# Kernel optimization log

Hardware: AMD Instinct MI355X
Metric: run time of the kernel (lower is better)

## Reference

```python
import jax, jax.numpy as jnp
import numpy as np

GAMMA = 1.0  # init arg gamma


def setup_inputs() -> dict:
    key = jax.random.key(0)
    ks = jax.random.split(key, 7)
    Bn, C, C_, H = 8, 256, 32, 64
    sc = 1.0 / np.sqrt(C)
    return {
        "x_activation": jax.random.normal(ks[0], (Bn, C, H, H), dtype=jnp.float32),
        "f_w": jax.random.normal(ks[1], (C_, C), dtype=jnp.float32) * sc,
        "f_b": jnp.zeros((C_,), dtype=jnp.float32),
        "g_w": jax.random.normal(ks[2], (C_, C), dtype=jnp.float32) * sc,
        "g_b": jnp.zeros((C_,), dtype=jnp.float32),
        "h_w": jax.random.normal(ks[3], (C, C), dtype=jnp.float32) * sc,
        "h_b": jnp.zeros((C,), dtype=jnp.float32),
    }


def reference(x_activation, f_w, f_b, g_w, g_b, h_w, h_b):
    Bn, C, H, W = x_activation.shape
    N = H * W
    xf = x_activation.reshape(Bn, C, N)  # [B, C, N]
    # 1x1 convs are per-pixel linear maps over channels
    f = jnp.einsum('oc,bcn->bon', f_w, xf) + f_b[:, None]  # [B, C_, N]
    g = jnp.einsum('oc,bcn->bon', g_w, xf) + g_b[:, None]  # [B, C_, N]
    h = jnp.einsum('oc,bcn->bon', h_w, xf) + h_b[:, None]  # [B, C, N]
    # S[b, i, j] = sum_c f[b, c, i] * g[b, c, j]  (f^T @ g), shape [B, N, N]
    S = jnp.einsum('bci,bcj->bij', f, g)
    # NOTE: original uses Softmax(dim=1) -> normalize over the i (query/f) axis
    B = jax.nn.softmax(S, axis=1)
    # O (post-transpose) [b, c, i] = sum_j B[b, i, j] * h[b, c, j]
    O = jnp.einsum('bij,bcj->bci', B, h).reshape(Bn, C, H, W)
    return GAMMA * O + x_activation
```

## Files before the change

### kernel.cpp

```cpp
#include <hip/hip_runtime.h>
#include <hip/hip_fp16.h>
#include <cmath>


#define BN 8
#define CC 256
#define CQ 32
#define NN 4096

typedef _Float16 half8 __attribute__((ext_vector_type(8)));
typedef _Float16 half4v __attribute__((ext_vector_type(4)));
typedef float f32x4 __attribute__((ext_vector_type(4)));

static __device__ __forceinline__ float fexp2(float x) {
    return __builtin_amdgcn_exp2f(x);
}

#define LOG2E 1.44269504f
#define SHIFT2 28.8539008f

__global__ __launch_bounds__(256) void transpose_kernel(
    const float* __restrict__ x, __half* __restrict__ xt,
    const float* __restrict__ fw, const float* __restrict__ gw,
    const float* __restrict__ hw, __half* __restrict__ wf16)
{
    const int gid = blockIdx.x;

    if (gid >= 2048) {
        int i = (gid - 2048) * 256 + threadIdx.x;
        float v;
        if (i < 8192)       v = fw[i];
        else if (i < 16384) v = gw[i - 8192];
        else                v = hw[i - 16384];
        wf16[i] = __float2half(v);
        return;
    }

    const int b = gid & 7, rest = gid >> 3;
    const int n0 = (rest & 63) * 64;
    const int c0 = (rest >> 6) * 64;
    const int tid = threadIdx.x;

    __shared__ float T[64 * 65];

    const float* xb = x + ((size_t)b * CC + c0) * NN + n0;
    const int u  = tid >> 4;
    const int n4 = (tid & 15) * 4;
#pragma unroll
    for (int r = 0; r < 4; ++r) {
        int c = r * 16 + u;
        f32x4 v = __builtin_nontemporal_load((const f32x4*)(xb + (size_t)c * NN + n4));
        T[c * 65 + n4 + 0] = v.x;
        T[c * 65 + n4 + 1] = v.y;
        T[c * 65 + n4 + 2] = v.z;
        T[c * 65 + n4 + 3] = v.w;
    }
    __syncthreads();

    const int lane = tid & 63, w = tid >> 6;
    const int n  = w * 16 + (lane >> 2);
    const int cc = (lane & 3) * 16;
    half8 o0, o1;
#pragma unroll
    for (int k = 0; k < 8; ++k) {
        o0[k] = (_Float16)T[(cc + k) * 65 + n];
        o1[k] = (_Float16)T[(cc + 8 + k) * 65 + n];
    }
    __half* dst = xt + ((size_t)b * NN + n0 + n) * CC + c0 + cc;
    *(half8*)(void*)dst = o0;
    *(half8*)(void*)(dst + 8) = o1;
}

__global__ __launch_bounds__(256) void proj_kernel(
    const __half* __restrict__ xt, const __half* __restrict__ wf16,
    const float* __restrict__ fb, const float* __restrict__ gb,
    const float* __restrict__ hb,
    __half* __restrict__ ft, __half* __restrict__ gt, __half* __restrict__ hm)
{
    const int tid = threadIdx.x;
    const int w = tid >> 6, lane = tid & 63, col = lane & 15, q = lane >> 4;
    const int gid = blockIdx.x;
    const int b = gid & 7, rest = gid >> 3;
    const int n0 = (rest & 63) * 64;
    const int ot = rest >> 6;

    const __half* xtb  = xt + (size_t)b * NN * CC;
    const __half* fw16 = wf16;
    const __half* gw16 = wf16 + 8192;
    const __half* hw16 = wf16 + 16384;

    f32x4 acc[4];
#pragma unroll
    for (int mt = 0; mt < 4; ++mt) acc[mt] = (f32x4){0.f, 0.f, 0.f, 0.f};

    if (ot == 0) {
        const int pix = n0 + 16 * w + col;
#pragma unroll
        for (int ks = 0; ks < 8; ++ks) {
            half8 bf = *(const half8*)(const void*)(xtb + (size_t)pix * CC + ks * 32 + q * 8);
#pragma unroll
            for (int mt = 0; mt < 4; ++mt) {
                const __half* wp = (mt < 2) ? (fw16 + (16 * mt + col) * CC)
                                            : (gw16 + (16 * (mt - 2) + col) * CC);
                half8 af = *(const half8*)(const void*)(wp + ks * 32 + q * 8);
                acc[mt] = __builtin_amdgcn_mfma_f32_16x16x32_f16(af, bf, acc[mt], 0, 0, 0);
            }
        }
#pragma unroll
        for (int mt = 0; mt < 4; ++mt) {
            const int mtl = mt & 1;
            const float* bsel = (mt < 2) ? fb : gb;
            __half* dsel = (mt < 2) ? ft : gt;
            half4v hv;
#pragma unroll
            for (int r = 0; r < 4; ++r)
                hv[r] = (_Float16)(acc[mt][r] + bsel[16 * mtl + 4 * q + r]);
            *(half4v*)(void*)(dsel + ((size_t)b * NN + pix) * CQ + 16 * mtl + 4 * q) = hv;
        }
    } else {
        const int c = (ot - 1) * 64 + 16 * w + col;
#pragma unroll
        for (int ks = 0; ks < 8; ++ks) {
            half8 bf = *(const half8*)(const void*)(hw16 + (size_t)c * CC + ks * 32 + q * 8);
#pragma unroll
            for (int mt = 0; mt < 4; ++mt) {
                half8 af = *(const half8*)(const void*)(xtb + (size_t)(n0 + 16 * mt + col) * CC + ks * 32 + q * 8);
                acc[mt] = __builtin_amdgcn_mfma_f32_16x16x32_f16(af, bf, acc[mt], 0, 0, 0);
            }
        }
        const float bias = hb[c];
#pragma unroll
        for (int mt = 0; mt < 4; ++mt) {
            half4v hv;
#pragma unroll
            for (int r = 0; r < 4; ++r)
                hv[r] = (_Float16)(acc[mt][r] + bias);
            *(half4v*)(void*)(hm + ((size_t)b * CC + c) * NN + n0 + 16 * mt + 4 * q) = hv;
        }
    }
}

__global__ __launch_bounds__(256) void pass1_kernel(
    const __half* __restrict__ ft, const __half* __restrict__ gt,
    float* __restrict__ shl)
{
    const int tid = threadIdx.x;
    const int w = tid >> 6, lane = tid & 63, col = lane & 15, q = lane >> 4;
    const int gid = blockIdx.x;
    const int b = gid & 7;
    const int jg = (gid >> 3) * 64 + 16 * w + col;

    const __half* fbase = ft + (size_t)b * NN * CQ;
    half8 gfrag = *(const half8*)(const void*)(gt + ((size_t)b * NN + jg) * CQ + q * 8);

    float a0 = 0.f, a1 = 0.f, a2 = 0.f, a3 = 0.f;
    const f32x4 zero = {0.f, 0.f, 0.f, 0.f};

    half8 a_cur = *(const half8*)(const void*)(fbase + (size_t)col * CQ + q * 8);
    for (int i0 = 0; i0 < NN; i0 += 16) {
        int i_n = (i0 + 16) & (NN - 1);
        half8 a_next = *(const half8*)(const void*)(fbase + (size_t)(i_n + col) * CQ + q * 8);
        f32x4 d = __builtin_amdgcn_mfma_f32_16x16x32_f16(a_cur, gfrag, zero, 0, 0, 0);
        a0 += fexp2(fmaf(d[0], LOG2E, -SHIFT2));
        a1 += fexp2(fmaf(d[1], LOG2E, -SHIFT2));
        a2 += fexp2(fmaf(d[2], LOG2E, -SHIFT2));
        a3 += fexp2(fmaf(d[3], LOG2E, -SHIFT2));
        a_cur = a_next;
    }
    float l = (a0 + a1) + (a2 + a3);
    l += __shfl_xor(l, 16);
    l += __shfl_xor(l, 32);
    if (q == 0)
        shl[(size_t)b * NN + jg] = -__log2f(l) - SHIFT2;
}

__global__ __launch_bounds__(512, 4) void pass2_kernel(
    const float* __restrict__ x,
    const __half* __restrict__ ft, const __half* __restrict__ gt,
    const __half* __restrict__ hm, const float* __restrict__ shl,
    float* __restrict__ out)
{
    const int tid = threadIdx.x;
    const int w = tid >> 6, lane = tid & 63, col = lane & 15, q = lane >> 4;
    const int gid = blockIdx.x;
    const int b  = gid & 7;
    const int i0 = (gid >> 3) * 64;
    const int sg  = w >> 2;
    const int sw4 = w & 3;
    const int cb  = 32 * w;

    __shared__ __half P[2][64 * 64];

    const __half* gbase = gt + (size_t)b * NN * CQ;
    const __half* hbase = hm + (size_t)b * CC * NN;
    const float*  lb    = shl + (size_t)b * NN;

    half8 ffr[4];
#pragma unroll
    for (int it = 0; it < 4; ++it)
        ffr[it] = *(const half8*)(const void*)(ft + ((size_t)b * NN + i0 + 16 * it + col) * CQ + q * 8);

    const __half* hrow[2];
#pragma unroll
    for (int ns = 0; ns < 2; ++ns)
        hrow[ns] = hbase + (size_t)(cb + 16 * ns + col) * NN + q * 8;

    f32x4 acc[4][2];
#pragma unroll
    for (int it = 0; it < 4; ++it)
#pragma unroll
        for (int ns = 0; ns < 2; ++ns)
            acc[it][ns] = (f32x4){0.f, 0.f, 0.f, 0.f};

    const f32x4 zero = {0.f, 0.f, 0.f, 0.f};
    const int sw  = 8 * (col & 7);
    const int jsl = 16 * sw4 + 4 * q;

    half8 gfr = *(const half8*)(const void*)(
        gbase + (size_t)(sg * 64 + 16 * sw4 + col) * CQ + q * 8);

    if (sg == 0) {
        f32x4 sl = *(const f32x4*)(lb + jsl);
        f32x4 d[4];
#pragma unroll
        for (int it = 0; it < 4; ++it)
            d[it] = __builtin_amdgcn_mfma_f32_16x16x32_f16(gfr, ffr[it], zero, 0, 0, 0);
        gfr = *(const half8*)(const void*)(
            gbase + (size_t)(128 + 16 * sw4 + col) * CQ + q * 8);
#pragma unroll
        for (int it = 0; it < 4; ++it) {
            half4v pv;
#pragma unroll
            for (int r = 0; r < 4; ++r)
                pv[r] = (_Float16)fexp2(fmaf(d[it][r], LOG2E, sl[r]));
            *(half4v*)(void*)(&P[0][0] + (16 * it + col) * 64 + (jsl ^ sw)) = pv;
        }
    }
    __syncthreads();

    for (int t = 0; t < 64; ++t) {
        const int j0 = t * 64;
        const __half* Pr = &P[t & 1][0];

        half8 hv[2][2];
#pragma unroll
        for (int ns = 0; ns < 2; ++ns)
#pragma unroll
            for (int ks = 0; ks < 2; ++ks)
                hv[ns][ks] = *(const half8*)(const void*)(hrow[ns] + j0 + ks * 32);

        const bool duty = (((t + 1) & 1) == sg) && (t < 63);
        f32x4 d[4];
        f32x4 sl;
        if (duty) {
            sl = *(const f32x4*)(lb + (t + 1) * 64 + jsl);
#pragma unroll
            for (int it = 0; it < 4; ++it)
                d[it] = __builtin_amdgcn_mfma_f32_16x16x32_f16(gfr, ffr[it], zero, 0, 0, 0);
            const int rn = (t + 3) & 63;
            gfr = *(const half8*)(const void*)(
                gbase + (size_t)(rn * 64 + 16 * sw4 + col) * CQ + q * 8);
        }

        __builtin_amdgcn_s_setprio(1);
#pragma unroll
        for (int ks = 0; ks < 2; ++ks) {
            half8 af[4];
#pragma unroll
            for (int it = 0; it < 4; ++it)
                af[it] = *(const half8*)(const void*)(
                    Pr + (16 * it + col) * 64 + ((ks * 32 + q * 8) ^ sw));
#pragma unroll
            for (int it = 0; it < 4; ++it)
#pragma unroll
                for (int ns = 0; ns < 2; ++ns)
                    acc[it][ns] = __builtin_amdgcn_mfma_f32_16x16x32_f16(
                        af[it], hv[ns][ks], acc[it][ns], 0, 0, 0);
        }
        __builtin_amdgcn_s_setprio(0);

        if (duty) {
            __half* Pw = &P[(t + 1) & 1][0];
#pragma unroll
            for (int it = 0; it < 4; ++it) {
                half4v pv;
#pragma unroll
                for (int r = 0; r < 4; ++r)
                    pv[r] = (_Float16)fexp2(fmaf(d[it][r], LOG2E, sl[r]));
                *(half4v*)(void*)(Pw + (16 * it + col) * 64 + (jsl ^ sw)) = pv;
            }
        }
        __syncthreads();
    }

    const float* xb = x + (size_t)b * CC * NN;
    float* ob = out + (size_t)b * CC * NN;
#pragma unroll
    for (int it = 0; it < 4; ++it) {
#pragma unroll
        for (int ns = 0; ns < 2; ++ns) {
            int c  = cb + 16 * ns + col;
            int ii = i0 + 16 * it + 4 * q;
            size_t off = (size_t)c * NN + ii;
            f32x4 xv = __builtin_nontemporal_load((const f32x4*)(xb + off));
            f32x4 ov;
            ov.x = acc[it][ns][0] + xv.x;
            ov.y = acc[it][ns][1] + xv.y;
            ov.z = acc[it][ns][2] + xv.z;
            ov.w = acc[it][ns][3] + xv.w;
            __builtin_nontemporal_store(ov, (f32x4*)(ob + off));
        }
    }
}

extern "C" void kernel_launch(void* const* d_in, const int* in_sizes, int n_in,
                              void* d_out, int out_size, void* d_ws, size_t ws_size,
                              hipStream_t stream)
{
    const float* x  = (const float*)d_in[0];
    const float* fw = (const float*)d_in[1];
    const float* fb = (const float*)d_in[2];
    const float* gw = (const float*)d_in[3];
    const float* gb = (const float*)d_in[4];
    const float* hw = (const float*)d_in[5];
    const float* hb = (const float*)d_in[6];
    float* out = (float*)d_out;

    char* ws = (char*)d_ws;
    __half* xt = (__half*)(ws);
    __half* wf = (__half*)(ws + (size_t)16777216);
    __half* ft = (__half*)(ws + (size_t)17039360);
    __half* gt = (__half*)(ws + (size_t)19136512);
    __half* hm = (__half*)(ws + (size_t)21233664);
    float*  lv = (float*) (ws + (size_t)38010880);

    transpose_kernel<<<dim3(2368), dim3(256), 0, stream>>>(x, xt, fw, gw, hw, wf);
    proj_kernel<<<dim3(2560), dim3(256), 0, stream>>>(xt, wf, fb, gb, hb, ft, gt, hm);
    pass1_kernel<<<dim3(512), dim3(256), 0, stream>>>(ft, gt, lv);
    pass2_kernel<<<dim3(512), dim3(512), 0, stream>>>(x, ft, gt, hm, lv, out);
}
```

Baseline: 331.2 us.

## Spread softmax tile work across all warps and prefetch h fragments one step ahead

In pass2, the P-tile computation for the next step moves from one half of the warps on alternating steps to all eight warps every step, each doing two of the four 16-row sub-tiles. This balances exp/MFMA work per iteration. The h fragments for the next j-tile are now loaded a full iteration ahead into registers to hide global-memory latency, at the cost of extra VGPRs. Pass1's score loop is also unrolled by two so two MFMAs and their loads are in flight together.

```diff
diff --git a/kernel.cpp b/kernel.cpp
--- a/kernel.cpp
+++ b/kernel.cpp
@@ -156,16 +156,20 @@
     float a0 = 0.f, a1 = 0.f, a2 = 0.f, a3 = 0.f;
     const f32x4 zero = {0.f, 0.f, 0.f, 0.f};
 
-    half8 a_cur = *(const half8*)(const void*)(fbase + (size_t)col * CQ + q * 8);
-    for (int i0 = 0; i0 < NN; i0 += 16) {
-        int i_n = (i0 + 16) & (NN - 1);
-        half8 a_next = *(const half8*)(const void*)(fbase + (size_t)(i_n + col) * CQ + q * 8);
-        f32x4 d = __builtin_amdgcn_mfma_f32_16x16x32_f16(a_cur, gfrag, zero, 0, 0, 0);
-        a0 += fexp2(fmaf(d[0], LOG2E, -SHIFT2));
-        a1 += fexp2(fmaf(d[1], LOG2E, -SHIFT2));
-        a2 += fexp2(fmaf(d[2], LOG2E, -SHIFT2));
-        a3 += fexp2(fmaf(d[3], LOG2E, -SHIFT2));
-        a_cur = a_next;
+    half8 a0v = *(const half8*)(const void*)(fbase + (size_t)col * CQ + q * 8);
+    half8 a1v = *(const half8*)(const void*)(fbase + (size_t)(16 + col) * CQ + q * 8);
+    for (int i0 = 0; i0 < NN; i0 += 32) {
+        int i_n = (i0 + 32) & (NN - 1);
+        half8 a2v = *(const half8*)(const void*)(fbase + (size_t)(i_n + col) * CQ + q * 8);
+        half8 a3v = *(const half8*)(const void*)(fbase + (size_t)(i_n + 16 + col) * CQ + q * 8);
+        f32x4 d0 = __builtin_amdgcn_mfma_f32_16x16x32_f16(a0v, gfrag, zero, 0, 0, 0);
+        f32x4 d1 = __builtin_amdgcn_mfma_f32_16x16x32_f16(a1v, gfrag, zero, 0, 0, 0);
+        a0 += fexp2(fmaf(d0[0], LOG2E, -SHIFT2)) + fexp2(fmaf(d1[0], LOG2E, -SHIFT2));
+        a1 += fexp2(fmaf(d0[1], LOG2E, -SHIFT2)) + fexp2(fmaf(d1[1], LOG2E, -SHIFT2));
+        a2 += fexp2(fmaf(d0[2], LOG2E, -SHIFT2)) + fexp2(fmaf(d1[2], LOG2E, -SHIFT2));
+        a3 += fexp2(fmaf(d0[3], LOG2E, -SHIFT2)) + fexp2(fmaf(d1[3], LOG2E, -SHIFT2));
+        a0v = a2v;
+        a1v = a3v;
     }
     float l = (a0 + a1) + (a2 + a3);
     l += __shfl_xor(l, 16);
@@ -185,9 +189,9 @@
     const int gid = blockIdx.x;
     const int b  = gid & 7;
     const int i0 = (gid >> 3) * 64;
-    const int sg  = w >> 2;
-    const int sw4 = w & 3;
-    const int cb  = 32 * w;
+    const int ih = w >> 2;
+    const int jq = w & 3;
+    const int cb = 32 * w;
 
     __shared__ __half P[2][64 * 64];
 
@@ -195,10 +199,11 @@
     const __half* hbase = hm + (size_t)b * CC * NN;
     const float*  lb    = shl + (size_t)b * NN;
 
-    half8 ffr[4];
-#pragma unroll
-    for (int it = 0; it < 4; ++it)
-        ffr[it] = *(const half8*)(const void*)(ft + ((size_t)b * NN + i0 + 16 * it + col) * CQ + q * 8);
+    half8 ffr2[2];
+#pragma unroll
+    for (int t2 = 0; t2 < 2; ++t2)
+        ffr2[t2] = *(const half8*)(const void*)(
+            ft + ((size_t)b * NN + i0 + 16 * (2 * ih + t2) + col) * CQ + q * 8);
 
     const __half* hrow[2];
 #pragma unroll
@@ -214,53 +219,60 @@
 
     const f32x4 zero = {0.f, 0.f, 0.f, 0.f};
     const int sw  = 8 * (col & 7);
-    const int jsl = 16 * sw4 + 4 * q;
+    const int jsl = 16 * jq + 4 * q;
 
     half8 gfr = *(const half8*)(const void*)(
-        gbase + (size_t)(sg * 64 + 16 * sw4 + col) * CQ + q * 8);
-
-    if (sg == 0) {
-        f32x4 sl = *(const f32x4*)(lb + jsl);
-        f32x4 d[4];
-#pragma unroll
-        for (int it = 0; it < 4; ++it)
-            d[it] = __builtin_amdgcn_mfma_f32_16x16x32_f16(gfr, ffr[it], zero, 0, 0, 0);
+        gbase + (size_t)(16 * jq + col) * CQ + q * 8);
+
+    {
+        f32x4 sl0 = *(const f32x4*)(lb + jsl);
+        f32x4 d0[2];
+#pragma unroll
+        for (int t2 = 0; t2 < 2; ++t2)
+            d0[t2] = __builtin_amdgcn_mfma_f32_16x16x32_f16(gfr, ffr2[t2], zero, 0, 0, 0);
         gfr = *(const half8*)(const void*)(
-            gbase + (size_t)(128 + 16 * sw4 + col) * CQ + q * 8);
-#pragma unroll
-        for (int it = 0; it < 4; ++it) {
+            gbase + (size_t)(64 + 16 * jq + col) * CQ + q * 8);
+#pragma unroll
+        for (int t2 = 0; t2 < 2; ++t2) {
             half4v pv;
 #pragma unroll
             for (int r = 0; r < 4; ++r)
-                pv[r] = (_Float16)fexp2(fmaf(d[it][r], LOG2E, sl[r]));
-            *(half4v*)(void*)(&P[0][0] + (16 * it + col) * 64 + (jsl ^ sw)) = pv;
-        }
-    }
+                pv[r] = (_Float16)fexp2(fmaf(d0[t2][r], LOG2E, sl0[r]));
+            *(half4v*)(void*)(&P[0][0] + (16 * (2 * ih + t2) + col) * 64 + (jsl ^ sw)) = pv;
+        }
+    }
+    half8 hv[2][2];
+#pragma unroll
+    for (int ns = 0; ns < 2; ++ns)
+#pragma unroll
+        for (int ks = 0; ks < 2; ++ks)
+            hv[ns][ks] = *(const half8*)(const void*)(hrow[ns] + ks * 32);
     __syncthreads();
 
     for (int t = 0; t < 64; ++t) {
         const int j0 = t * 64;
         const __half* Pr = &P[t & 1][0];
-
-        half8 hv[2][2];
-#pragma unroll
-        for (int ns = 0; ns < 2; ++ns)
-#pragma unroll
-            for (int ks = 0; ks < 2; ++ks)
-                hv[ns][ks] = *(const half8*)(const void*)(hrow[ns] + j0 + ks * 32);
-
-        const bool duty = (((t + 1) & 1) == sg) && (t < 63);
-        f32x4 d[4];
+        const bool duty = (t < 63);
+
+        f32x4 d2[2];
         f32x4 sl;
         if (duty) {
             sl = *(const f32x4*)(lb + (t + 1) * 64 + jsl);
 #pragma unroll
-            for (int it = 0; it < 4; ++it)
-                d[it] = __builtin_amdgcn_mfma_f32_16x16x32_f16(gfr, ffr[it], zero, 0, 0, 0);
-            const int rn = (t + 3) & 63;
+            for (int t2 = 0; t2 < 2; ++t2)
+                d2[t2] = __builtin_amdgcn_mfma_f32_16x16x32_f16(gfr, ffr2[t2], zero, 0, 0, 0);
+            const int rn = (t + 2) & 63;
             gfr = *(const half8*)(const void*)(
-                gbase + (size_t)(rn * 64 + 16 * sw4 + col) * CQ + q * 8);
-        }
+                gbase + (size_t)(rn * 64 + 16 * jq + col) * CQ + q * 8);
+        }
+
+        const int jn = (j0 + 64) & (NN - 1);
+        half8 hv_n[2][2];
+#pragma unroll
+        for (int ns = 0; ns < 2; ++ns)
+#pragma unroll
+            for (int ks = 0; ks < 2; ++ks)
+                hv_n[ns][ks] = *(const half8*)(const void*)(hrow[ns] + jn + ks * 32);
 
         __builtin_amdgcn_s_setprio(1);
 #pragma unroll
@@ -282,15 +294,21 @@
         if (duty) {
             __half* Pw = &P[(t + 1) & 1][0];
 #pragma unroll
-            for (int it = 0; it < 4; ++it) {
+            for (int t2 = 0; t2 < 2; ++t2) {
                 half4v pv;
 #pragma unroll
                 for (int r = 0; r < 4; ++r)
-                    pv[r] = (_Float16)fexp2(fmaf(d[it][r], LOG2E, sl[r]));
-                *(half4v*)(void*)(Pw + (16 * it + col) * 64 + (jsl ^ sw)) = pv;
+                    pv[r] = (_Float16)fexp2(fmaf(d2[t2][r], LOG2E, sl[r]));
+                *(half4v*)(void*)(Pw + (16 * (2 * ih + t2) + col) * 64 + (jsl ^ sw)) = pv;
             }
         }
         __syncthreads();
+
+#pragma unroll
+        for (int ns = 0; ns < 2; ++ns)
+#pragma unroll
+            for (int ks = 0; ks < 2; ++ks)
+                hv[ns][ks] = hv_n[ns][ks];
     }
 
     const float* xb = x + (size_t)b * CC * NN;
```

After: 329.5 us. No clear change (-0.5%).
